# Performance work log

Measured on AMD Instinct MI355X. Metric: run time of the kernel, lower is better.

Reference implementation:

```python
import jax, jax.numpy as jnp
import numpy as np

K = 8
DIM = 128
NUM_BLOCKS = 12


def knn_idx(query, ref, k):
    # query (b,m,3), ref (b,n,3) -> idx (b,m,k) of k nearest refs per query
    d2 = (jnp.sum(query * query, -1)[:, :, None]
          + jnp.sum(ref * ref, -1)[:, None, :]
          - 2.0 * jnp.einsum('bmc,bnc->bmn', query, ref))
    _, idx = jax.lax.top_k(-d2, k)
    return idx


def gather(points, idx):
    # points (b,n,d), idx (b,m,k) -> (b,m,k,d)
    b = points.shape[0]
    return points[jnp.arange(b)[:, None, None], idx]


def feature_net(xyz, w0, w1, w2, k):
    # xyz (b,n,3); self-kNN relative coords then shared MLP, max over neighbors
    idx = knn_idx(xyz, xyz, k)
    grouped = gather(xyz, idx) - xyz[:, :, None, :]      # (b,n,k,3)
    out = jax.nn.relu(jnp.einsum('bnkc,cd->bnkd', grouped, w0))
    out = jax.nn.relu(jnp.einsum('bnkd,de->bnke', out, w1))
    out = jax.nn.relu(jnp.einsum('bnkd,de->bnke', out, w2))
    return jnp.max(out, axis=2)                          # (b,n,dim)


def res_graph_conv_unpool(xyz, points, wc, wn, uc, un, k):
    # xyz (b,n,3), points (b,n,d); wc/wn (12,d,d), uc/un (d,6)
    b, n, _ = xyz.shape
    idx = knn_idx(xyz, xyz, k)
    new_xyz = None
    for i in range(NUM_BLOCKS):
        shortcut = points
        p = jax.nn.relu(points)
        grouped = gather(p, idx)                         # (b,n,k,d)
        center = jnp.einsum('bnd,de->bne', p, wc[i])
        neigh = jnp.einsum('bnkd,de->bne', grouped, wn[i])  # summed over k
        points = (center + neigh) / float(k + 1) + shortcut  # mean over cat(1+k)
        if i == NUM_BLOCKS - 1:
            cx = jnp.einsum('bnd,de->bne', p, uc)        # (b,n,6)
            nx = jnp.einsum('bnkd,de->bne', grouped, un)
            off = (cx + nx) / float(k + 1)               # (b,n,6)
            # torch (b,6,n).view(b,3,2,n): channel j*2+r -> coord j, replica r
            off = off.reshape(b, n, 3, 2)
            off = jnp.transpose(off, (0, 3, 1, 2))       # (b,2,n,3)
            new_xyz = (xyz[:, None, :, :] + off).reshape(b, 2 * n, 3)
    return new_xyz, points


def setup_inputs() -> dict:
    key = jax.random.key(0)
    ks = jax.random.split(key, 12)
    s3 = 1.0 / np.sqrt(3.0)
    sd = 1.0 / np.sqrt(float(DIM))
    return {
        'xyz': jax.random.normal(ks[0], (4, 3, 4096), jnp.float32),
        'fn_w0': jax.random.normal(ks[1], (3, DIM), jnp.float32) * s3,
        'fn_w1': jax.random.normal(ks[2], (DIM, DIM), jnp.float32) * sd,
        'fn_w2': jax.random.normal(ks[3], (DIM, DIM), jnp.float32) * sd,
        'u1_wc': jax.random.normal(ks[4], (NUM_BLOCKS, DIM, DIM), jnp.float32) * sd,
        'u1_wn': jax.random.normal(ks[5], (NUM_BLOCKS, DIM, DIM), jnp.float32) * sd,
        'u1_uc': jax.random.normal(ks[6], (DIM, 6), jnp.float32) * sd,
        'u1_un': jax.random.normal(ks[7], (DIM, 6), jnp.float32) * sd,
        'u2_wc': jax.random.normal(ks[8], (NUM_BLOCKS, DIM, DIM), jnp.float32) * sd,
        'u2_wn': jax.random.normal(ks[9], (NUM_BLOCKS, DIM, DIM), jnp.float32) * sd,
        'u2_uc': jax.random.normal(ks[10], (DIM, 6), jnp.float32) * sd,
        'u2_un': jax.random.normal(ks[11], (DIM, 6), jnp.float32) * sd,
    }


def reference(xyz, fn_w0, fn_w1, fn_w2, u1_wc, u1_wn, u1_uc, u1_un,
              u2_wc, u2_wn, u2_uc, u2_un):
    x = jnp.transpose(xyz, (0, 2, 1))                    # (b,n,3)
    points = feature_net(x, fn_w0, fn_w1, fn_w2, K)      # (b,n,dim)
    new_xyz, points = res_graph_conv_unpool(x, points, u1_wc, u1_wn, u1_uc, u1_un, K)
    # kNN of each new point among the original points, gather + mean
    idx = knn_idx(new_xyz, x, K)                         # (b,2n,k)
    points = jnp.mean(gather(points, idx), axis=2)       # (b,2n,dim)
    new_xyz2, _ = res_graph_conv_unpool(new_xyz, points, u2_wc, u2_wn, u2_uc, u2_un, K)
    return jnp.transpose(new_xyz2, (0, 2, 1))            # (b,3,4n)
```

## Files before the change

### kernel.cpp

```cpp
#include <hip/hip_runtime.h>

#define NB 12

typedef __attribute__((ext_vector_type(8))) short bf16x8;
typedef __attribute__((ext_vector_type(4))) float f32x4;

#define MFMA16(a, b, c) __builtin_amdgcn_mfma_f32_16x16x32_bf16(a, b, c, 0, 0, 0)

__device__ __forceinline__ unsigned short bf16r(float f) {
  unsigned int u = __float_as_uint(f);
  return (unsigned short)((u + 0x7fffu + ((u >> 16) & 1u)) >> 16);
}

__device__ __forceinline__ float bf2f(unsigned short h) {
  return __uint_as_float(((unsigned int)h) << 16);
}

__device__ __forceinline__ float4 relu4(float4 v) {
  v.x = fmaxf(v.x, 0.f); v.y = fmaxf(v.y, 0.f);
  v.z = fmaxf(v.z, 0.f); v.w = fmaxf(v.w, 0.f);
  return v;
}

__device__ __forceinline__ void split8(float4 a, float4 b, bf16x8* ph, bf16x8* pl) {
  float v[8] = {a.x, a.y, a.z, a.w, b.x, b.y, b.z, b.w};
  bf16x8 h, l;
#pragma unroll
  for (int i = 0; i < 8; i++) {
    unsigned short hh = bf16r(v[i]);
    h[i] = (short)hh;
    l[i] = (short)bf16r(v[i] - bf2f(hh));
  }
  *ph = h; *pl = l;
}

__global__ __launch_bounds__(256) void k_transpose_in(
    const float* __restrict__ xyz, float* __restrict__ x, int n) {
  int gid = blockIdx.x * 256 + threadIdx.x;
  if (gid >= 4 * n) return;
  int b = gid / n, i = gid % n;
  const float* src = xyz + (size_t)b * 3 * n;
  float* dst = x + (size_t)gid * 3;
  dst[0] = src[i];
  dst[1] = src[n + i];
  dst[2] = src[2 * n + i];
}

__global__ __launch_bounds__(256) void k_wt(
    const float* __restrict__ wc, const float* __restrict__ wn,
    unsigned short* __restrict__ wth, unsigned short* __restrict__ wtl, int total) {
  int tid = blockIdx.x * 256 + threadIdx.x;
  if (tid >= total) return;
  int i = tid >> 15;
  int rem = tid & 32767;
  int e = rem >> 8, d = rem & 255;
  float v = (d < 128) ? wc[i * 16384 + d * 128 + e]
                      : wn[i * 16384 + (d - 128) * 128 + e];
  unsigned short h = bf16r(v);
  wth[tid] = h;
  wtl[tid] = bf16r(v - bf2f(h));
}

__global__ __launch_bounds__(256) void k_frag(
    const float* __restrict__ pts, unsigned short* __restrict__ frag, int n) {
  int gid = blockIdx.x * 256 + threadIdx.x;
  int ntiles = n >> 4;
  if (gid >= 4 * ntiles * 64) return;
  int lane = gid & 63;
  int bt = gid >> 6;
  int b = bt / ntiles, tile = bt % ntiles;
  int rin = lane & 15, kg = lane >> 4;
  const float* p = pts + ((size_t)b * n + tile * 16 + rin) * 3;
  float px = p[0], py = p[1], pz = p[2];
  float rr = px * px + py * py + pz * pz;
  unsigned short h0 = bf16r(px), h1 = bf16r(py), h2 = bf16r(pz);
  unsigned short l0 = bf16r(px - bf2f(h0));
  unsigned short l1 = bf16r(py - bf2f(h1));
  unsigned short l2 = bf16r(pz - bf2f(h2));
  unsigned short rh = bf16r(rr), rl = bf16r(rr - bf2f(rh));
  bf16x8 f = (bf16x8)0;
  if (kg == 0) {
    f[0] = (short)h0; f[1] = (short)h1; f[2] = (short)h2;
    f[3] = (short)l0; f[4] = (short)l1; f[5] = (short)l2;
    f[6] = (short)h0; f[7] = (short)h1;
  } else if (kg == 1) {
    f[0] = (short)h2; f[1] = (short)rh; f[2] = (short)rl;
  }
  *(bf16x8*)(frag + (size_t)gid * 8) = f;
}

#define LCAS(A, B)                                                        \
  {                                                                       \
    bool sw_ = (dist[B] < dist[A]) ||                                     \
               (dist[B] == dist[A] && ind[B] < ind[A]);                   \
    float td_ = sw_ ? dist[A] : dist[B];                                  \
    int ti_ = sw_ ? ind[A] : ind[B];                                      \
    dist[A] = sw_ ? dist[B] : dist[A];                                    \
    ind[A] = sw_ ? ind[B] : ind[A];                                      \
    dist[B] = td_; ind[B] = ti_;                                          \
  }

__global__ __launch_bounds__(256) void k_knn2(
    const float* __restrict__ Q, const float* __restrict__ Rpts,
    const unsigned short* __restrict__ frag,
    int* __restrict__ idx, int M, int N) {
  __shared__ unsigned short chunkbuf[32 * 512];
  __shared__ float smd[4][16][8];
  __shared__ int smi[4][16][8];
  int b = blockIdx.y;
  int t = threadIdx.x;
  int w = t >> 6, lane = t & 63;
  int col = lane & 15, kg = lane >> 4;
  int qg = w & 1, zh = w >> 1;
  int q = blockIdx.x * 32 + qg * 16 + col;
  const float* qp = Q + ((size_t)b * M + q) * 3;
  float qx = qp[0], qy = qp[1], qz = qp[2];
  float qq = qx * qx + qy * qy + qz * qz;
  float m2x = -2.f * qx, m2y = -2.f * qy, m2z = -2.f * qz;
  unsigned short h0 = bf16r(m2x), h1 = bf16r(m2y), h2 = bf16r(m2z);
  unsigned short l0 = bf16r(m2x - bf2f(h0));
  unsigned short l1 = bf16r(m2y - bf2f(h1));
  unsigned short l2 = bf16r(m2z - bf2f(h2));
  bf16x8 bfrag = (bf16x8)0;
  if (kg == 0) {
    bfrag[0] = (short)h0; bfrag[1] = (short)h1; bfrag[2] = (short)h2;
    bfrag[3] = (short)h0; bfrag[4] = (short)h1; bfrag[5] = (short)h2;
    bfrag[6] = (short)l0; bfrag[7] = (short)l1;
  } else if (kg == 1) {
    bfrag[0] = (short)l2;
    bfrag[1] = (short)0x3F80; bfrag[2] = (short)0x3F80;
  }
  float dist[8];
  int ind[8];
#pragma unroll
  for (int j = 0; j < 8; j++) { dist[j] = 3.4e38f; ind[j] = 0; }
  int ntiles = N >> 4;
  int half = ntiles >> 1;
  const unsigned short* fb = frag + (size_t)b * ntiles * 512;
  for (int c = 0; c < half; c += 16) {
    __syncthreads();
    {
      const float4* src = (const float4*)fb;
      float4* dst = (float4*)chunkbuf;
      for (int i = t; i < 2048; i += 256) {
        int tile = i >> 6, within = i & 63;
        int gt = (tile < 16) ? (c + tile) : (half + c + (tile - 16));
        dst[i] = src[(size_t)gt * 64 + within];
      }
    }
    __syncthreads();
    int lbase = zh * 16;
    int cbase = (zh * half + c) * 16;
#pragma unroll 4
    for (int tl = 0; tl < 16; tl++) {
      bf16x8 af = *(const bf16x8*)(&chunkbuf[((lbase + tl) * 64 + lane) * 8]);
      f32x4 z = (f32x4){0.f, 0.f, 0.f, 0.f};
      f32x4 sc = MFMA16(af, bfrag, z);
      float mn = fminf(fminf(sc[0], sc[1]), fminf(sc[2], sc[3]));
      if (mn < dist[7]) {
        int ibase = cbase + tl * 16 + kg * 4;
#pragma unroll
        for (int r = 0; r < 4; r++) {
          float dd = sc[r];
          if (dd < dist[7]) {
            int ii = ibase + r;
#pragma unroll
            for (int j = 0; j < 8; j++) {
              bool sw = dd < dist[j];
              float td = sw ? dist[j] : dd;
              int ti = sw ? ind[j] : ii;
              dist[j] = sw ? dd : dist[j];
              ind[j] = sw ? ii : ind[j];
              dd = td; ii = ti;
            }
          }
        }
      }
    }
  }
  {
    const float* Rb2 = Rpts + (size_t)b * N * 3;
    float nd[8];
#pragma unroll
    for (int j = 0; j < 8; j++) {
      int ii = ind[j];
      float rx = Rb2[(size_t)ii * 3 + 0];
      float ry = Rb2[(size_t)ii * 3 + 1];
      float rz = Rb2[(size_t)ii * 3 + 2];
      float rr = rx * rx + ry * ry + rz * rz;
      nd[j] = qq + rr - 2.0f * (qx * rx + qy * ry + qz * rz);
    }
    float sd[8]; int si[8];
#pragma unroll
    for (int j = 0; j < 8; j++) { sd[j] = 3.4e38f; si[j] = 0x7fffffff; }
#pragma unroll
    for (int j = 0; j < 8; j++) {
      float dd = nd[j]; int ii = ind[j];
#pragma unroll
      for (int p = 0; p < 8; p++) {
        bool sw = (dd < sd[p]) || (dd == sd[p] && ii < si[p]);
        float td = sw ? sd[p] : dd;
        int ti = sw ? si[p] : ii;
        sd[p] = sw ? dd : sd[p];
        si[p] = sw ? ii : si[p];
        dd = td; ii = ti;
      }
    }
#pragma unroll
    for (int j = 0; j < 8; j++) { dist[j] = sd[j]; ind[j] = si[j]; }
  }
#pragma unroll
  for (int lev = 0; lev < 2; lev++) {
    int D = 16 << lev;
    float od[8]; int oi[8];
#pragma unroll
    for (int j = 0; j < 8; j++) {
      od[j] = __shfl_xor(dist[j], D, 64);
      oi[j] = __shfl_xor(ind[j], D, 64);
    }
#pragma unroll
    for (int j = 0; j < 8; j++) {
      float bd = od[7 - j]; int bi = oi[7 - j];
      bool take = (bd < dist[j]) || (bd == dist[j] && bi < ind[j]);
      dist[j] = take ? bd : dist[j];
      ind[j] = take ? bi : ind[j];
    }
    LCAS(0, 4) LCAS(1, 5) LCAS(2, 6) LCAS(3, 7)
    LCAS(0, 2) LCAS(1, 3) LCAS(4, 6) LCAS(5, 7)
    LCAS(0, 1) LCAS(2, 3) LCAS(4, 5) LCAS(6, 7)
  }
  if (kg == 0) {
#pragma unroll
    for (int j = 0; j < 8; j++) { smd[w][col][j] = dist[j]; smi[w][col][j] = ind[j]; }
  }
  __syncthreads();
  int tq = t >> 3, jj = t & 7;
  int g = tq >> 4, qcol = tq & 15;
  float d0 = smd[g][qcol][jj];     int i0 = smi[g][qcol][jj];
  float d1 = smd[g + 2][qcol][jj]; int i1 = smi[g + 2][qcol][jj];
  int r0 = jj, r1 = jj;
#pragma unroll
  for (int p = 0; p < 8; p++) {
    float dp = smd[g + 2][qcol][p]; int ip = smi[g + 2][qcol][p];
    r0 += (dp < d0 || (dp == d0 && ip < i0)) ? 1 : 0;
    float dq = smd[g][qcol][p];     int iq = smi[g][qcol][p];
    r1 += (dq < d1 || (dq == d1 && iq < i1)) ? 1 : 0;
  }
  int* o = idx + ((size_t)b * M + blockIdx.x * 32 + tq) * 8;
  if (r0 < 8) o[r0] = i0;
  if (r1 < 8) o[r1] = i1;
}

__global__ __launch_bounds__(256) void k_featnet(
    const float* __restrict__ x, const int* __restrict__ idx,
    const float* __restrict__ w0, const float* __restrict__ w1,
    const float* __restrict__ w2, float* __restrict__ out, int n) {
  __shared__ float X0[64][128];
  __shared__ float X1[64][128];
  int b = blockIdx.y;
  int q0 = blockIdx.x * 8;
  int t = threadIdx.x;
  {
    int row = t >> 2, seg = t & 3;
    int qi = row >> 3, j = row & 7;
    size_t qb = (size_t)b * n + (q0 + qi);
    const float* qp = x + qb * 3;
    int nb = idx[qb * 8 + j];
    const float* pp = x + ((size_t)b * n + nb) * 3;
    float r0 = pp[0] - qp[0], r1 = pp[1] - qp[1], r2 = pp[2] - qp[2];
    int c0 = seg * 32;
#pragma unroll
    for (int u = 0; u < 8; u++) {
      int cc = c0 + u * 4;
      float4 a = *(const float4*)(w0 + cc);
      float4 bb = *(const float4*)(w0 + 128 + cc);
      float4 cv = *(const float4*)(w0 + 256 + cc);
      float4 h;
      h.x = fmaxf(fmaf(r0, a.x, fmaf(r1, bb.x, r2 * cv.x)), 0.f);
      h.y = fmaxf(fmaf(r0, a.y, fmaf(r1, bb.y, r2 * cv.y)), 0.f);
      h.z = fmaxf(fmaf(r0, a.z, fmaf(r1, bb.z, r2 * cv.z)), 0.f);
      h.w = fmaxf(fmaf(r0, a.w, fmaf(r1, bb.w, r2 * cv.w)), 0.f);
      *(float4*)(&X0[row][cc]) = h;
    }
  }
  __syncthreads();
  int rg = t >> 5, cg = t & 31;
  int r0r = rg * 8, c0 = cg * 4;
  float acc[8][4];
#pragma unroll
  for (int i = 0; i < 8; i++)
#pragma unroll
    for (int c = 0; c < 4; c++) acc[i][c] = 0.f;
  for (int e = 0; e < 128; e++) {
    float4 w = *(const float4*)(w1 + e * 128 + c0);
#pragma unroll
    for (int i = 0; i < 8; i++) {
      float xi = X0[r0r + i][e];
      acc[i][0] = fmaf(xi, w.x, acc[i][0]);
      acc[i][1] = fmaf(xi, w.y, acc[i][1]);
      acc[i][2] = fmaf(xi, w.z, acc[i][2]);
      acc[i][3] = fmaf(xi, w.w, acc[i][3]);
    }
  }
#pragma unroll
  for (int i = 0; i < 8; i++) {
    float4 h;
    h.x = fmaxf(acc[i][0], 0.f); h.y = fmaxf(acc[i][1], 0.f);
    h.z = fmaxf(acc[i][2], 0.f); h.w = fmaxf(acc[i][3], 0.f);
    *(float4*)(&X1[r0r + i][c0]) = h;
  }
  __syncthreads();
#pragma unroll
  for (int i = 0; i < 8; i++)
#pragma unroll
    for (int c = 0; c < 4; c++) acc[i][c] = 0.f;
  for (int e = 0; e < 128; e++) {
    float4 w = *(const float4*)(w2 + e * 128 + c0);
#pragma unroll
    for (int i = 0; i < 8; i++) {
      float xi = X1[r0r + i][e];
      acc[i][0] = fmaf(xi, w.x, acc[i][0]);
      acc[i][1] = fmaf(xi, w.y, acc[i][1]);
      acc[i][2] = fmaf(xi, w.z, acc[i][2]);
      acc[i][3] = fmaf(xi, w.w, acc[i][3]);
    }
  }
  float4 m; m.x = 0.f; m.y = 0.f; m.z = 0.f; m.w = 0.f;
#pragma unroll
  for (int i = 0; i < 8; i++) {
    m.x = fmaxf(m.x, acc[i][0]); m.y = fmaxf(m.y, acc[i][1]);
    m.z = fmaxf(m.z, acc[i][2]); m.w = fmaxf(m.w, acc[i][3]);
  }
  *(float4*)(out + ((size_t)b * n + q0 + rg) * 128 + c0) = m;
}

__global__ __launch_bounds__(256) void k_conv(
    const float* __restrict__ Pin, float* __restrict__ Pout,
    const int* __restrict__ idx, const unsigned short* __restrict__ wth,
    const unsigned short* __restrict__ wtl, int n) {
  __shared__ unsigned short Xh[64 * 256];
  __shared__ unsigned short Xl[64 * 256];
  int b = blockIdx.y, t = threadIdx.x;
  int rblk = blockIdx.x * 64;
  {
    int row = t >> 2, seg = t & 3;
    size_t rb = (size_t)b * n + rblk + row;
    const float4* src = (const float4*)(Pin + rb * 128 + seg * 32);
    float4 cv[8];
#pragma unroll
    for (int u = 0; u < 8; u++) cv[u] = relu4(src[u]);
    const int* ip = idx + rb * 8;
    float4 ns[8];
#pragma unroll
    for (int u = 0; u < 8; u++) ns[u] = make_float4(0.f, 0.f, 0.f, 0.f);
#pragma unroll
    for (int j = 0; j < 8; j++) {
      const float4* s2 = (const float4*)(Pin + ((size_t)b * n + ip[j]) * 128 + seg * 32);
#pragma unroll
      for (int u = 0; u < 8; u++) {
        float4 v = relu4(s2[u]);
        ns[u].x += v.x; ns[u].y += v.y; ns[u].z += v.z; ns[u].w += v.w;
      }
    }
#pragma unroll
    for (int u = 0; u < 4; u++) {
      int lc = seg * 4 + u;
      int ph = (row * 256 + ((lc ^ (row & 7)) * 8));
      split8(cv[2 * u], cv[2 * u + 1], (bf16x8*)&Xh[ph], (bf16x8*)&Xl[ph]);
      int lc2 = 16 + seg * 4 + u;
      int ph2 = (row * 256 + ((lc2 ^ (row & 7)) * 8));
      split8(ns[2 * u], ns[2 * u + 1], (bf16x8*)&Xh[ph2], (bf16x8*)&Xl[ph2]);
    }
  }
  __syncthreads();
  int w = t >> 6, lane = t & 63;
  int lo = lane & 15, hi = lane >> 4;
  f32x4 acc[4][2];
#pragma unroll
  for (int mt = 0; mt < 4; mt++)
#pragma unroll
    for (int nt = 0; nt < 2; nt++) acc[mt][nt] = (f32x4){0.f, 0.f, 0.f, 0.f};
  const unsigned short* wbh = wth + ((size_t)(w * 32 + lo) * 256 + hi * 8);
  const unsigned short* wbl = wtl + ((size_t)(w * 32 + lo) * 256 + hi * 8);
#pragma unroll
  for (int kk = 0; kk < 8; kk++) {
    bf16x8 ah[4], al[4];
#pragma unroll
    for (int mt = 0; mt < 4; mt++) {
      int row = mt * 16 + lo;
      int off = row * 256 + (((4 * kk + hi) ^ (row & 7)) * 8);
      ah[mt] = *(const bf16x8*)(&Xh[off]);
      al[mt] = *(const bf16x8*)(&Xl[off]);
    }
    bf16x8 bh0 = *(const bf16x8*)(wbh + kk * 32);
    bf16x8 bh1 = *(const bf16x8*)(wbh + 4096 + kk * 32);
    bf16x8 bl0 = *(const bf16x8*)(wbl + kk * 32);
    bf16x8 bl1 = *(const bf16x8*)(wbl + 4096 + kk * 32);
#pragma unroll
    for (int mt = 0; mt < 4; mt++) {
      acc[mt][0] = MFMA16(ah[mt], bh0, acc[mt][0]);
      acc[mt][0] = MFMA16(ah[mt], bl0, acc[mt][0]);
      acc[mt][0] = MFMA16(al[mt], bh0, acc[mt][0]);
      acc[mt][1] = MFMA16(ah[mt], bh1, acc[mt][1]);
      acc[mt][1] = MFMA16(ah[mt], bl1, acc[mt][1]);
      acc[mt][1] = MFMA16(al[mt], bh1, acc[mt][1]);
    }
  }
  const float inv9 = 1.0f / 9.0f;
#pragma unroll
  for (int mt = 0; mt < 4; mt++)
#pragma unroll
    for (int nt = 0; nt < 2; nt++) {
      int col = w * 32 + nt * 16 + lo;
#pragma unroll
      for (int r = 0; r < 4; r++) {
        int row = rblk + mt * 16 + hi * 4 + r;
        size_t off = ((size_t)b * n + row) * 128 + col;
        Pout[off] = fmaf(acc[mt][nt][r], inv9, Pin[off]);
      }
    }
}

__global__ __launch_bounds__(256) void k_unpool(
    const float* __restrict__ Pin, const int* __restrict__ idx,
    const float* __restrict__ xin,
    const float* __restrict__ uc, const float* __restrict__ un,
    float* __restrict__ out, int n, int transposed) {
  int b = blockIdx.y;
  int wv = threadIdx.x >> 6, lane = threadIdx.x & 63;
  int i = blockIdx.x * 4 + wv;
  if (i >= n) return;
  size_t rb = (size_t)b * n + i;
  const float* p0 = Pin + rb * 128;
  float pd0 = fmaxf(p0[lane], 0.f), pd1 = fmaxf(p0[lane + 64], 0.f);
  const int* ip = idx + rb * 8;
  float ns0 = 0.f, ns1 = 0.f;
#pragma unroll
  for (int j = 0; j < 8; j++) {
    const float* pj = Pin + ((size_t)b * n + ip[j]) * 128;
    ns0 += fmaxf(pj[lane], 0.f);
    ns1 += fmaxf(pj[lane + 64], 0.f);
  }
  float acc[6];
#pragma unroll
  for (int o = 0; o < 6; o++)
    acc[o] = pd0 * uc[lane * 6 + o] + pd1 * uc[(lane + 64) * 6 + o] +
             ns0 * un[lane * 6 + o] + ns1 * un[(lane + 64) * 6 + o];
#pragma unroll
  for (int s = 32; s > 0; s >>= 1) {
#pragma unroll
    for (int o = 0; o < 6; o++) acc[o] += __shfl_xor(acc[o], s, 64);
  }
  if (lane < 6) {
    int j = lane >> 1, r = lane & 1;
    float v = xin[rb * 3 + j] + acc[lane] * (1.0f / 9.0f);
    if (transposed)
      out[(size_t)b * 6 * n + (size_t)j * 2 * n + (size_t)r * n + i] = v;
    else
      out[((size_t)b * 2 * n + (size_t)r * n + i) * 3 + j] = v;
  }
}

__global__ __launch_bounds__(256) void k_meangather(
    const float* __restrict__ Pin, const int* __restrict__ idx,
    float* __restrict__ Pout, int M, int nsrc) {
  int gid = blockIdx.x * 256 + threadIdx.x;
  int row = gid >> 6, lane = gid & 63;
  if (row >= 4 * M) return;
  int b = row / M;
  const int* ip = idx + (size_t)row * 8;
  float s0 = 0.f, s1 = 0.f;
#pragma unroll
  for (int j = 0; j < 8; j++) {
    const float* p = Pin + ((size_t)b * nsrc + ip[j]) * 128;
    s0 += p[lane];
    s1 += p[lane + 64];
  }
  Pout[(size_t)row * 128 + lane] = s0 * 0.125f;
  Pout[(size_t)row * 128 + lane + 64] = s1 * 0.125f;
}

extern "C" void kernel_launch(void* const* d_in, const int* in_sizes, int n_in,
                              void* d_out, int out_size, void* d_ws, size_t ws_size,
                              hipStream_t stream) {
  const float* xyz = (const float*)d_in[0];
  const float* fw0 = (const float*)d_in[1];
  const float* fw1 = (const float*)d_in[2];
  const float* fw2 = (const float*)d_in[3];
  const float* u1wc = (const float*)d_in[4];
  const float* u1wn = (const float*)d_in[5];
  const float* u1uc = (const float*)d_in[6];
  const float* u1un = (const float*)d_in[7];
  const float* u2wc = (const float*)d_in[8];
  const float* u2wn = (const float*)d_in[9];
  const float* u2uc = (const float*)d_in[10];
  const float* u2un = (const float*)d_in[11];
  float* out = (float*)d_out;

  const int n1 = 4096, n2 = 8192, B = 4;
  float* ws = (float*)d_ws;
  float* x = ws;
  float* nxz = x + (size_t)B * n1 * 3;
  int* idx1 = (int*)(nxz + (size_t)B * n2 * 3);
  int* idx2g = idx1 + (size_t)B * n1 * 8;
  int* idx2s = idx2g + (size_t)B * n2 * 8;
  float* A = (float*)(idx2s + (size_t)B * n2 * 8);
  float* Bb = A + (size_t)B * n2 * 128;
  unsigned short* wt1h = (unsigned short*)(Bb + (size_t)B * n2 * 128);
  unsigned short* wt1l = wt1h + (size_t)NB * 128 * 256;
  unsigned short* wt2h = wt1l + (size_t)NB * 128 * 256;
  unsigned short* wt2l = wt2h + (size_t)NB * 128 * 256;
  unsigned short* fragx = wt2l + (size_t)NB * 128 * 256;
  unsigned short* fragn = fragx + (size_t)B * (n1 / 16) * 512;

  const int wtot = NB * 128 * 256;
  k_wt<<<dim3((wtot + 255) / 256), 256, 0, stream>>>(u1wc, u1wn, wt1h, wt1l, wtot);
  k_wt<<<dim3((wtot + 255) / 256), 256, 0, stream>>>(u2wc, u2wn, wt2h, wt2l, wtot);

  k_transpose_in<<<dim3((B * n1 + 255) / 256), 256, 0, stream>>>(xyz, x, n1);
  k_frag<<<dim3(B * (n1 / 16) * 64 / 256), 256, 0, stream>>>(x, fragx, n1);
  k_knn2<<<dim3(n1 / 32, B), 256, 0, stream>>>(x, x, fragx, idx1, n1, n1);
  k_featnet<<<dim3(n1 / 8, B), 256, 0, stream>>>(x, idx1, fw0, fw1, fw2, A, n1);
  for (int i = 0; i < NB; i++) {
    const float* pin = (i & 1) ? Bb : A;
    float* pout = (i & 1) ? A : Bb;
    k_conv<<<dim3(n1 / 64, B), 256, 0, stream>>>(
        pin, pout, idx1, wt1h + (size_t)i * 128 * 256, wt1l + (size_t)i * 128 * 256, n1);
  }
  k_unpool<<<dim3(n1 / 4, B), 256, 0, stream>>>(Bb, idx1, x, u1uc, u1un, nxz, n1, 0);
  k_frag<<<dim3(B * (n2 / 16) * 64 / 256), 256, 0, stream>>>(nxz, fragn, n2);
  k_knn2<<<dim3(n2 / 32, B), 256, 0, stream>>>(nxz, x, fragx, idx2g, n2, n1);
  k_meangather<<<dim3((B * n2 * 64 + 255) / 256), 256, 0, stream>>>(A, idx2g, Bb, n2, n1);
  k_knn2<<<dim3(n2 / 32, B), 256, 0, stream>>>(nxz, nxz, fragn, idx2s, n2, n2);
  for (int i = 0; i < NB; i++) {
    const float* pin = (i & 1) ? A : Bb;
    float* pout = (i & 1) ? Bb : A;
    k_conv<<<dim3(n2 / 64, B), 256, 0, stream>>>(
        pin, pout, idx2s, wt2h + (size_t)i * 128 * 256, wt2l + (size_t)i * 128 * 256, n2);
  }
  k_unpool<<<dim3(n2 / 4, B), 256, 0, stream>>>(A, idx2s, nxz, u2uc, u2un, out, n2, 1);
}
```

Baseline: 1.297 ms.

## Halve conv row tile and use wave-wide kNN candidate insertion with shared threshold

k_conv now processes 32 rows per block instead of 64, with 8 threads per row. This halves LDS and register use per block and doubles the grid, which should raise occupancy and spread the memory-bound gather over more blocks. k_knn2 replaces the nested per-element insertion with a bitmask of candidates. Lanes drain that mask in a wave-uniform loop, and the threshold is tightened after each chunk by a cross-lane min of the 8th-best distance. The chunk copy loop is also simplified to two contiguous copies. The cost is more blocks re-reading weights and an extra shuffle reduction per chunk.

New measurement: 1.302 ms. No clear change (+0.3%).

```diff
diff --git a/kernel.cpp b/kernel.cpp
--- a/kernel.cpp
+++ b/kernel.cpp
@@ -134,6 +134,7 @@
   int ind[8];
 #pragma unroll
   for (int j = 0; j < 8; j++) { dist[j] = 3.4e38f; ind[j] = 0; }
+  float g8 = 3.4e38f;
   int ntiles = N >> 4;
   int half = ntiles >> 1;
   const unsigned short* fb = frag + (size_t)b * ntiles * 512;
@@ -142,41 +143,45 @@
     {
       const float4* src = (const float4*)fb;
       float4* dst = (float4*)chunkbuf;
-      for (int i = t; i < 2048; i += 256) {
-        int tile = i >> 6, within = i & 63;
-        int gt = (tile < 16) ? (c + tile) : (half + c + (tile - 16));
-        dst[i] = src[(size_t)gt * 64 + within];
+      for (int i = t; i < 1024; i += 256) {
+        dst[i] = src[(size_t)c * 64 + i];
+        dst[1024 + i] = src[(size_t)(half + c) * 64 + i];
       }
     }
     __syncthreads();
     int lbase = zh * 16;
     int cbase = (zh * half + c) * 16;
-#pragma unroll 4
     for (int tl = 0; tl < 16; tl++) {
       bf16x8 af = *(const bf16x8*)(&chunkbuf[((lbase + tl) * 64 + lane) * 8]);
       f32x4 z = (f32x4){0.f, 0.f, 0.f, 0.f};
       f32x4 sc = MFMA16(af, bfrag, z);
-      float mn = fminf(fminf(sc[0], sc[1]), fminf(sc[2], sc[3]));
-      if (mn < dist[7]) {
-        int ibase = cbase + tl * 16 + kg * 4;
-#pragma unroll
-        for (int r = 0; r < 4; r++) {
-          float dd = sc[r];
-          if (dd < dist[7]) {
-            int ii = ibase + r;
-#pragma unroll
-            for (int j = 0; j < 8; j++) {
-              bool sw = dd < dist[j];
-              float td = sw ? dist[j] : dd;
-              int ti = sw ? ind[j] : ii;
-              dist[j] = sw ? dd : dist[j];
-              ind[j] = sw ? ii : ind[j];
-              dd = td; ii = ti;
-            }
+      float g = fminf(dist[7], g8);
+      unsigned int m = 0;
+      m |= (sc[0] < g) ? 1u : 0u;
+      m |= (sc[1] < g) ? 2u : 0u;
+      m |= (sc[2] < g) ? 4u : 0u;
+      m |= (sc[3] < g) ? 8u : 0u;
+      while (__any(m != 0u)) {
+        if (m != 0u) {
+          int r = (int)__builtin_ctz(m);
+          m &= m - 1u;
+          float dd = (r & 2) ? ((r & 1) ? sc[3] : sc[2])
+                             : ((r & 1) ? sc[1] : sc[0]);
+          int ii = cbase + tl * 16 + kg * 4 + r;
+#pragma unroll
+          for (int j = 0; j < 8; j++) {
+            bool sw = dd < dist[j];
+            float td = sw ? dist[j] : dd;
+            int ti = sw ? ind[j] : ii;
+            dist[j] = sw ? dd : dist[j];
+            ind[j] = sw ? ii : ind[j];
+            dd = td; ii = ti;
           }
         }
       }
     }
+    float t1 = fminf(dist[7], __shfl_xor(dist[7], 16, 64));
+    g8 = fminf(t1, __shfl_xor(t1, 32, 64));
   }
   {
     const float* Rb2 = Rpts + (size_t)b * N * 3;
@@ -338,36 +343,36 @@
     const float* __restrict__ Pin, float* __restrict__ Pout,
     const int* __restrict__ idx, const unsigned short* __restrict__ wth,
     const unsigned short* __restrict__ wtl, int n) {
-  __shared__ unsigned short Xh[64 * 256];
-  __shared__ unsigned short Xl[64 * 256];
+  __shared__ unsigned short Xh[32 * 256];
+  __shared__ unsigned short Xl[32 * 256];
   int b = blockIdx.y, t = threadIdx.x;
-  int rblk = blockIdx.x * 64;
+  int rblk = blockIdx.x * 32;
   {
-    int row = t >> 2, seg = t & 3;
+    int row = t >> 3, seg = t & 7;
     size_t rb = (size_t)b * n + rblk + row;
-    const float4* src = (const float4*)(Pin + rb * 128 + seg * 32);
-    float4 cv[8];
-#pragma unroll
-    for (int u = 0; u < 8; u++) cv[u] = relu4(src[u]);
+    const float4* src = (const float4*)(Pin + rb * 128 + seg * 16);
+    float4 cv[4];
+#pragma unroll
+    for (int u = 0; u < 4; u++) cv[u] = relu4(src[u]);
     const int* ip = idx + rb * 8;
-    float4 ns[8];
-#pragma unroll
-    for (int u = 0; u < 8; u++) ns[u] = make_float4(0.f, 0.f, 0.f, 0.f);
+    float4 ns[4];
+#pragma unroll
+    for (int u = 0; u < 4; u++) ns[u] = make_float4(0.f, 0.f, 0.f, 0.f);
 #pragma unroll
     for (int j = 0; j < 8; j++) {
-      const float4* s2 = (const float4*)(Pin + ((size_t)b * n + ip[j]) * 128 + seg * 32);
-#pragma unroll
-      for (int u = 0; u < 8; u++) {
+      const float4* s2 = (const float4*)(Pin + ((size_t)b * n + ip[j]) * 128 + seg * 16);
+#pragma unroll
+      for (int u = 0; u < 4; u++) {
         float4 v = relu4(s2[u]);
         ns[u].x += v.x; ns[u].y += v.y; ns[u].z += v.z; ns[u].w += v.w;
       }
     }
 #pragma unroll
-    for (int u = 0; u < 4; u++) {
-      int lc = seg * 4 + u;
+    for (int u = 0; u < 2; u++) {
+      int lc = seg * 2 + u;
       int ph = (row * 256 + ((lc ^ (row & 7)) * 8));
       split8(cv[2 * u], cv[2 * u + 1], (bf16x8*)&Xh[ph], (bf16x8*)&Xl[ph]);
-      int lc2 = 16 + seg * 4 + u;
+      int lc2 = 16 + seg * 2 + u;
       int ph2 = (row * 256 + ((lc2 ^ (row & 7)) * 8));
       split8(ns[2 * u], ns[2 * u + 1], (bf16x8*)&Xh[ph2], (bf16x8*)&Xl[ph2]);
     }
@@ -375,18 +380,18 @@
   __syncthreads();
   int w = t >> 6, lane = t & 63;
   int lo = lane & 15, hi = lane >> 4;
-  f32x4 acc[4][2];
-#pragma unroll
-  for (int mt = 0; mt < 4; mt++)
+  f32x4 acc[2][2];
+#pragma unroll
+  for (int mt = 0; mt < 2; mt++)
 #pragma unroll
     for (int nt = 0; nt < 2; nt++) acc[mt][nt] = (f32x4){0.f, 0.f, 0.f, 0.f};
   const unsigned short* wbh = wth + ((size_t)(w * 32 + lo) * 256 + hi * 8);
   const unsigned short* wbl = wtl + ((size_t)(w * 32 + lo) * 256 + hi * 8);
 #pragma unroll
   for (int kk = 0; kk < 8; kk++) {
-    bf16x8 ah[4], al[4];
-#pragma unroll
-    for (int mt = 0; mt < 4; mt++) {
+    bf16x8 ah[2], al[2];
+#pragma unroll
+    for (int mt = 0; mt < 2; mt++) {
       int row = mt * 16 + lo;
       int off = row * 256 + (((4 * kk + hi) ^ (row & 7)) * 8);
       ah[mt] = *(const bf16x8*)(&Xh[off]);
@@ -397,7 +402,7 @@
     bf16x8 bl0 = *(const bf16x8*)(wbl + kk * 32);
     bf16x8 bl1 = *(const bf16x8*)(wbl + 4096 + kk * 32);
 #pragma unroll
-    for (int mt = 0; mt < 4; mt++) {
+    for (int mt = 0; mt < 2; mt++) {
       acc[mt][0] = MFMA16(ah[mt], bh0, acc[mt][0]);
       acc[mt][0] = MFMA16(ah[mt], bl0, acc[mt][0]);
       acc[mt][0] = MFMA16(al[mt], bh0, acc[mt][0]);
@@ -408,7 +413,7 @@
   }
   const float inv9 = 1.0f / 9.0f;
 #pragma unroll
-  for (int mt = 0; mt < 4; mt++)
+  for (int mt = 0; mt < 2; mt++)
 #pragma unroll
     for (int nt = 0; nt < 2; nt++) {
       int col = w * 32 + nt * 16 + lo;
@@ -524,7 +529,7 @@
   for (int i = 0; i < NB; i++) {
     const float* pin = (i & 1) ? Bb : A;
     float* pout = (i & 1) ? A : Bb;
-    k_conv<<<dim3(n1 / 64, B), 256, 0, stream>>>(
+    k_conv<<<dim3(n1 / 32, B), 256, 0, stream>>>(
         pin, pout, idx1, wt1h + (size_t)i * 128 * 256, wt1l + (size_t)i * 128 * 256, n1);
   }
   k_unpool<<<dim3(n1 / 4, B), 256, 0, stream>>>(Bb, idx1, x, u1uc, u1un, nxz, n1, 0);
@@ -535,7 +540,7 @@
   for (int i = 0; i < NB; i++) {
     const float* pin = (i & 1) ? A : Bb;
     float* pout = (i & 1) ? Bb : A;
-    k_conv<<<dim3(n2 / 64, B), 256, 0, stream>>>(
+    k_conv<<<dim3(n2 / 32, B), 256, 0, stream>>>(
         pin, pout, idx2s, wt2h + (size_t)i * 128 * 256, wt2l + (size_t)i * 128 * 256, n2);
   }
   k_unpool<<<dim3(n2 / 4, B), 256, 0, stream>>>(A, idx2s, nxz, u2uc, u2un, out, n2, 1);
```
